# Performance work log

Hardware: AMD Instinct MI355X
Metric: run time of the kernel (lower is better)

Reference implementation:

```python
import jax, jax.numpy as jnp
import numpy as np

EPS = 1e-6
H = 16; D_NOPE = 128; D_ROPE = 64; D_V = 128; D_QK = D_NOPE + D_ROPE
Q_RANK = 1536; KV_RANK = 512; HID = 2048


def rmsnorm(x, w):
    var = jnp.mean(jnp.square(x.astype(jnp.float32)), axis=-1, keepdims=True)
    return (x * jax.lax.rsqrt(var + EPS)).astype(x.dtype) * w


def rotate_half(x):
    x1, x2 = jnp.split(x, 2, axis=-1)
    return jnp.concatenate([-x2, x1], axis=-1)


def interleave(x):
    # deepseek interleaved rope: pairs (0,1),(2,3).. -> [evens | odds]
    b, h, s, d = x.shape
    return x.reshape(b, h, s, d // 2, 2).transpose(0, 1, 2, 4, 3).reshape(b, h, s, d)


def setup_inputs() -> dict:
    key = jax.random.key(0)
    ks = jax.random.split(key, 8)
    B, S = 2, 2048
    sc = lambda n: 1.0 / np.sqrt(n)
    inp = {
        'hidden_states': jax.random.normal(ks[0], (B, S, HID), jnp.float32),
        'w_qa': jax.random.normal(ks[1], (HID, Q_RANK), jnp.float32) * sc(HID),
        'g_qa': jnp.ones((Q_RANK,), jnp.float32),
        'w_qb': jax.random.normal(ks[2], (Q_RANK, H * D_QK), jnp.float32) * sc(Q_RANK),
        'w_kva': jax.random.normal(ks[3], (HID, KV_RANK + D_ROPE), jnp.float32) * sc(HID),
        'g_kva': jnp.ones((KV_RANK,), jnp.float32),
        'w_kvb': jax.random.normal(ks[4], (KV_RANK, H * (D_NOPE + D_V)), jnp.float32) * sc(KV_RANK),
        'w_o': jax.random.normal(ks[5], (H * D_V, HID), jnp.float32) * sc(H * D_V),
    }
    pos = jnp.arange(S, dtype=jnp.float32)
    inv = 1.0 / (10000.0 ** (jnp.arange(0, D_ROPE, 2, dtype=jnp.float32) / D_ROPE))
    emb = jnp.concatenate([pos[:, None] * inv[None, :]] * 2, axis=-1)  # [S, 64]
    inp['cos'] = jnp.broadcast_to(jnp.cos(emb)[None], (B, S, D_ROPE))
    inp['sin'] = jnp.broadcast_to(jnp.sin(emb)[None], (B, S, D_ROPE))
    return inp


def reference(hidden_states, w_qa, g_qa, w_qb, w_kva, g_kva, w_kvb, w_o, cos, sin):
    B, S, _ = hidden_states.shape
    scaling = D_QK ** -0.5
    # low-rank Q: q_b_proj(q_a_layernorm(q_a_proj(h)))
    q = rmsnorm(hidden_states @ w_qa, g_qa) @ w_qb
    q = q.reshape(B, S, H, D_QK).transpose(0, 2, 1, 3)          # [B,H,S,192]
    q_pass, q_rot = q[..., :D_NOPE], q[..., D_NOPE:]
    # compressed KV latent + shared rope key
    ckv = hidden_states @ w_kva                                  # [B,S,576]
    k_pass, k_rot = ckv[..., :KV_RANK], ckv[..., KV_RANK:]
    kv = rmsnorm(k_pass, g_kva) @ w_kvb                          # [B,S,H*256]
    kv = kv.reshape(B, S, H, D_NOPE + D_V).transpose(0, 2, 1, 3)
    k_nope, v = kv[..., :D_NOPE], kv[..., D_NOPE:]
    k_rot = k_rot.reshape(B, 1, S, D_ROPE)
    c = cos[:, None, :, :]; sn = sin[:, None, :, :]
    q_rot = interleave(q_rot); k_rot = interleave(k_rot)
    q_rot = q_rot * c + rotate_half(q_rot) * sn
    k_rot = k_rot * c + rotate_half(k_rot) * sn
    k_rot = jnp.broadcast_to(k_rot, (B, H, S, D_ROPE))
    qf = jnp.concatenate([q_pass, q_rot], axis=-1)               # [B,H,S,192]
    kf = jnp.concatenate([k_nope, k_rot], axis=-1)               # [B,H,S,192]
    scores = jnp.einsum('bhqd,bhkd->bhqk', qf, kf) * scaling
    mask = jnp.triu(jnp.full((S, S), jnp.finfo(jnp.float32).min, jnp.float32), 1)
    probs = jax.nn.softmax(scores.astype(jnp.float32) + mask, axis=-1).astype(qf.dtype)
    out = jnp.einsum('bhqk,bhkd->bhqd', probs, v)                # [B,H,S,128]
    out = out.transpose(0, 2, 1, 3).reshape(B, S, H * D_V)
    return out @ w_o
```

## Files before the change

kernel.cpp:

```cpp
#include <hip/hip_runtime.h>

#define DI __device__ __forceinline__

typedef __attribute__((ext_vector_type(8))) unsigned short u16x8;
typedef __attribute__((ext_vector_type(8))) __bf16 bf16x8;
typedef __attribute__((ext_vector_type(4))) float f32x4;

constexpr int B_ = 2, S_ = 2048, H_ = 16, HID_ = 2048;
constexpr int QR = 1536, KVR = 512, DQK = 192;
constexpr int BS = B_ * S_;
constexpr float SCALE = 0.07216878364870323f;
constexpr float QS = SCALE * 1.4426950408889634f;
constexpr int CKV_LD = 2176;

DI unsigned short f2bf(float x){
  unsigned r;
  asm("v_cvt_pk_bf16_f32 %0, %1, %2" : "=v"(r) : "v"(x), "v"(x));
  return (unsigned short)r;
}
DI float bf2f(unsigned short h){
  return __builtin_bit_cast(float, ((unsigned)h) << 16);
}
DI f32x4 mfma16(u16x8 a, u16x8 b, f32x4 c){
  return __builtin_amdgcn_mfma_f32_16x16x32_bf16(
      __builtin_bit_cast(bf16x8, a), __builtin_bit_cast(bf16x8, b), c, 0, 0, 0);
}
DI void async16(const void* g, void* l){
  __builtin_amdgcn_global_load_lds(
      (__attribute__((address_space(1))) void*)(g),
      (__attribute__((address_space(3))) void*)(l), 16, 0, 0);
}

__global__ __launch_bounds__(256) void cvt_f32_bf16(const float* __restrict__ in,
                                                    unsigned short* __restrict__ out, int n8){
  const int i = blockIdx.x * 256 + threadIdx.x;
  if (i >= n8) return;
  const float4* pp = (const float4*)in + (long)i * 2;
  float4 a = pp[0], b = pp[1];
  u16x8 r;
  r[0]=f2bf(a.x); r[1]=f2bf(a.y); r[2]=f2bf(a.z); r[3]=f2bf(a.w);
  r[4]=f2bf(b.x); r[5]=f2bf(b.y); r[6]=f2bf(b.z); r[7]=f2bf(b.w);
  *(u16x8*)(out + (long)i * 8) = r;
}

__global__ __launch_bounds__(256) void wtrans(const float* __restrict__ W,
                                              unsigned short* __restrict__ Wt,
                                              int K, int N, int Np){
  __shared__ float t[32][33];
  const int n0 = blockIdx.x * 32, k0 = blockIdx.y * 32;
  const int tid = threadIdx.x;
  const int c = tid & 31, r0 = tid >> 5;
  #pragma unroll
  for (int i = 0; i < 4; ++i){
    const int r = r0 + i * 8;
    float v = 0.f;
    if (n0 + c < N) v = W[(long)(k0 + r) * N + n0 + c];
    t[r][c] = v;
  }
  __syncthreads();
  #pragma unroll
  for (int i = 0; i < 4; ++i){
    const int r = r0 + i * 8;
    Wt[(long)(n0 + r) * K + k0 + c] = f2bf(t[c][r]);
  }
}

template<int COLS>
__global__ __launch_bounds__(256) void rmsnorm_k(const float* __restrict__ X, int ldx,
                                                 const float* __restrict__ g,
                                                 unsigned short* __restrict__ Y, int ldy){
  constexpr int PT = COLS / 256;
  const int row = blockIdx.x, tid = threadIdx.x;
  const float* xr = X + (long)row * ldx;
  float v[PT];
  float ss = 0.f;
  #pragma unroll
  for (int i = 0; i < PT; ++i){ v[i] = xr[tid + i * 256]; ss += v[i] * v[i]; }
  #pragma unroll
  for (int off = 32; off >= 1; off >>= 1) ss += __shfl_xor(ss, off);
  __shared__ float red[4];
  if ((tid & 63) == 0) red[tid >> 6] = ss;
  __syncthreads();
  const float tot = red[0] + red[1] + red[2] + red[3];
  const float rs = rsqrtf(tot / (float)COLS + 1e-6f);
  #pragma unroll
  for (int i = 0; i < PT; ++i)
    Y[(long)row * ldy + tid + i * 256] = f2bf(v[i] * rs * g[tid + i * 256]);
}

__global__ __launch_bounds__(256) void gemm_bt(const unsigned short* __restrict__ A,
                                               const unsigned short* __restrict__ Bt,
                                               float* __restrict__ C, int N, int K){
  __shared__ unsigned short lA[128 * 64];
  __shared__ unsigned short lB[128 * 64];
  const int tid = threadIdx.x;
  const int w = tid >> 6, lane = tid & 63, lr = lane & 15, lg = lane >> 4;
  const int wm = w >> 1, wn = w & 1;
  const long m0 = (long)blockIdx.y * 128, n0 = (long)blockIdx.x * 128;
  f32x4 acc[4][4] = {};
  const unsigned short* Ab = A + m0 * K;
  const unsigned short* Bb = Bt + n0 * K;
  for (int k0 = 0; k0 < K; k0 += 64){
    #pragma unroll
    for (int s2 = 0; s2 < 4; ++s2){
      const int c = s2 * 256 + tid;
      async16(Ab + (long)(c >> 3) * K + k0 + (c & 7) * 8, &lA[(s2 * 256 + w * 64) * 8]);
      async16(Bb + (long)(c >> 3) * K + k0 + (c & 7) * 8, &lB[(s2 * 256 + w * 64) * 8]);
    }
    __syncthreads();
    u16x8 a[2][4], b[2][4];
    #pragma unroll
    for (int kk = 0; kk < 2; ++kk){
      #pragma unroll
      for (int m = 0; m < 4; ++m)
        a[kk][m] = *(const u16x8*)&lA[(wm * 64 + m * 16 + lr) * 64 + kk * 32 + lg * 8];
      #pragma unroll
      for (int n = 0; n < 4; ++n)
        b[kk][n] = *(const u16x8*)&lB[(wn * 64 + n * 16 + lr) * 64 + kk * 32 + lg * 8];
    }
    #pragma unroll
    for (int kk = 0; kk < 2; ++kk)
      #pragma unroll
      for (int m = 0; m < 4; ++m)
        #pragma unroll
        for (int n = 0; n < 4; ++n)
          acc[m][n] = mfma16(a[kk][m], b[kk][n], acc[m][n]);
    __syncthreads();
  }
  #pragma unroll
  for (int m = 0; m < 4; ++m){
    const long row = m0 + wm * 64 + m * 16 + lg * 4;
    #pragma unroll
    for (int n = 0; n < 4; ++n){
      const long col = n0 + wn * 64 + n * 16 + lr;
      #pragma unroll
      for (int r = 0; r < 4; ++r)
        C[(row + r) * N + col] = acc[m][n][r];
    }
  }
}

__global__ __launch_bounds__(256) void gemm_qpack(const unsigned short* __restrict__ A,
                                                  const unsigned short* __restrict__ Bt,
                                                  const float* __restrict__ cosb,
                                                  const float* __restrict__ sinb,
                                                  unsigned short* __restrict__ qf, int K){
  const int N = 3072;
  __shared__ unsigned short lA[128 * 64];
  __shared__ unsigned short lB[128 * 64];
  const int tid = threadIdx.x;
  const int w = tid >> 6, lane = tid & 63, lr = lane & 15, lg = lane >> 4;
  const int wm = w >> 1, wn = w & 1;
  const long m0 = (long)blockIdx.y * 128, n0 = (long)blockIdx.x * 128;
  f32x4 acc[4][4] = {};
  const unsigned short* Ab = A + m0 * K;
  const unsigned short* Bb = Bt + n0 * K;
  for (int k0 = 0; k0 < K; k0 += 64){
    #pragma unroll
    for (int s2 = 0; s2 < 4; ++s2){
      const int c = s2 * 256 + tid;
      async16(Ab + (long)(c >> 3) * K + k0 + (c & 7) * 8, &lA[(s2 * 256 + w * 64) * 8]);
      async16(Bb + (long)(c >> 3) * K + k0 + (c & 7) * 8, &lB[(s2 * 256 + w * 64) * 8]);
    }
    __syncthreads();
    u16x8 a[2][4], b[2][4];
    #pragma unroll
    for (int kk = 0; kk < 2; ++kk){
      #pragma unroll
      for (int m = 0; m < 4; ++m)
        a[kk][m] = *(const u16x8*)&lA[(wm * 64 + m * 16 + lr) * 64 + kk * 32 + lg * 8];
      #pragma unroll
      for (int n = 0; n < 4; ++n)
        b[kk][n] = *(const u16x8*)&lB[(wn * 64 + n * 16 + lr) * 64 + kk * 32 + lg * 8];
    }
    #pragma unroll
    for (int kk = 0; kk < 2; ++kk)
      #pragma unroll
      for (int m = 0; m < 4; ++m)
        #pragma unroll
        for (int n = 0; n < 4; ++n)
          acc[m][n] = mfma16(a[kk][m], b[kk][n], acc[m][n]);
    __syncthreads();
  }
  #pragma unroll
  for (int m = 0; m < 4; ++m){
    const int rowg = (int)m0 + wm * 64 + m * 16 + lg * 4;
    #pragma unroll
    for (int n = 0; n < 4; ++n){
      const int col = (int)n0 + wn * 64 + n * 16 + lr;
      const int h = (unsigned)col / 192u;
      const int d = col - h * 192;
      #pragma unroll
      for (int r = 0; r < 4; ++r){
        const int rowi = rowg + r;
        const float a = acc[m][n][r];
        const float partner = __shfl_xor(a, 1);
        float val; int dout;
        if (d < 128){ val = a; dout = d; }
        else {
          const int ii = (d - 128) >> 1;
          const float c  = cosb[(long)rowi * 64 + ii];
          const float sn = sinb[(long)rowi * 64 + ii];
          val  = (d & 1) ? (a * c + partner * sn) : (a * c - partner * sn);
          dout = 128 + ((d & 1) << 5) + ii;
        }
        const int b = rowi >> 11, s = rowi & 2047;
        qf[((long)(b * 16 + h) * S_ + s) * DQK + dout] = f2bf(val * QS);
      }
    }
  }
}

__global__ __launch_bounds__(256) void gemm_kvpack(const unsigned short* __restrict__ A,
                                                   const unsigned short* __restrict__ Bt,
                                                   unsigned short* __restrict__ kf,
                                                   unsigned short* __restrict__ kvm, int K){
  const int N = 4096;
  __shared__ unsigned short lA[128 * 64];
  __shared__ unsigned short lB[128 * 64];
  const int tid = threadIdx.x;
  const int w = tid >> 6, lane = tid & 63, lr = lane & 15, lg = lane >> 4;
  const int wm = w >> 1, wn = w & 1;
  const long m0 = (long)blockIdx.y * 128, n0 = (long)blockIdx.x * 128;
  f32x4 acc[4][4] = {};
  const unsigned short* Ab = A + m0 * K;
  const unsigned short* Bb = Bt + n0 * K;
  for (int k0 = 0; k0 < K; k0 += 64){
    #pragma unroll
    for (int s2 = 0; s2 < 4; ++s2){
      const int c = s2 * 256 + tid;
      async16(Ab + (long)(c >> 3) * K + k0 + (c & 7) * 8, &lA[(s2 * 256 + w * 64) * 8]);
      async16(Bb + (long)(c >> 3) * K + k0 + (c & 7) * 8, &lB[(s2 * 256 + w * 64) * 8]);
    }
    __syncthreads();
    u16x8 a[2][4], b[2][4];
    #pragma unroll
    for (int kk = 0; kk < 2; ++kk){
      #pragma unroll
      for (int m = 0; m < 4; ++m)
        a[kk][m] = *(const u16x8*)&lA[(wm * 64 + m * 16 + lr) * 64 + kk * 32 + lg * 8];
      #pragma unroll
      for (int n = 0; n < 4; ++n)
        b[kk][n] = *(const u16x8*)&lB[(wn * 64 + n * 16 + lr) * 64 + kk * 32 + lg * 8];
    }
    #pragma unroll
    for (int kk = 0; kk < 2; ++kk)
      #pragma unroll
      for (int m = 0; m < 4; ++m)
        #pragma unroll
        for (int n = 0; n < 4; ++n)
          acc[m][n] = mfma16(a[kk][m], b[kk][n], acc[m][n]);
    __syncthreads();
  }
  #pragma unroll
  for (int m = 0; m < 4; ++m){
    const int rowg = (int)m0 + wm * 64 + m * 16 + lg * 4;
    #pragma unroll
    for (int n = 0; n < 4; ++n){
      const int col = (int)n0 + wn * 64 + n * 16 + lr;
      const int h = col >> 8, d = col & 255;
      #pragma unroll
      for (int r = 0; r < 4; ++r){
        const int rowi = rowg + r;
        const unsigned short v = f2bf(acc[m][n][r]);
        const int b = rowi >> 11, s = rowi & 2047;
        if (d < 128) kf[((long)(b * 16 + h) * S_ + s) * DQK + d] = v;
        else         kvm[(long)rowi * 4096 + col] = v;
      }
    }
  }
}

__global__ __launch_bounds__(256) void pack_krot(const float* __restrict__ ckv,
                                                 const float* __restrict__ cosb,
                                                 const float* __restrict__ sinb,
                                                 unsigned short* __restrict__ kf){
  const int row = blockIdx.x, tid = threadIdx.x;
  const int b = row >> 11, s = row & 2047;
  const float* cv = ckv + (long)row * CKV_LD + QR + KVR;
  const float* cr = cosb + (long)row * 64;
  const float* sr = sinb + (long)row * 64;
  #pragma unroll
  for (int j = 0; j < 4; ++j){
    const int o = j * 256 + tid;
    const int h = o >> 6, i = o & 63, ii = i & 31;
    const float e = cv[2 * ii], od = cv[2 * ii + 1];
    const float c = cr[ii], sn = sr[ii];
    const float val = (i < 32) ? (e * c - od * sn) : (od * c + e * sn);
    kf[((long)(b * 16 + h) * S_ + s) * DQK + 128 + i] = f2bf(val);
  }
}

__global__ __launch_bounds__(256) void pack_v(const unsigned short* __restrict__ kvm,
                                              unsigned short* __restrict__ vt){
  const int bh = blockIdx.x, s0 = blockIdx.y * 64;
  const int b = bh >> 4, h = bh & 15;
  __shared__ unsigned short t[64][130];
  #pragma unroll
  for (int it = 0; it < 32; ++it){
    const int idx = it * 256 + threadIdx.x;
    const int sl = idx >> 7, d = idx & 127;
    t[sl][d] = kvm[(long)(b * S_ + s0 + sl) * 4096 + h * 256 + 128 + d];
  }
  __syncthreads();
  #pragma unroll
  for (int it = 0; it < 32; ++it){
    const int idx = it * 256 + threadIdx.x;
    const int dr = idx >> 6, sc = idx & 63;
    vt[(long)(bh * 128 + dr) * S_ + s0 + sc] = t[sc][dr];
  }
}

__global__ __launch_bounds__(256) void mla_attn(const unsigned short* __restrict__ qf,
                                                const unsigned short* __restrict__ kf,
                                                const unsigned short* __restrict__ vt,
                                                unsigned short* __restrict__ ao){
  __shared__ unsigned short k_lds[2][64 * 192];
  __shared__ unsigned short v_lds[2][128 * 64];
  __shared__ unsigned short p_lds[4][32][72];
  const int bid = blockIdx.x;
  const int u = bid >> 5;
  const int qt = (u < 8) ? (15 - u) : (u - 8);
  const int bh = bid & 31;
  const int b = bh >> 4, h = bh & 15;
  const int tid = threadIdx.x;
  const int w = tid >> 6, lane = tid & 63, lr = lane & 15, lg = lane >> 4;
  const int q0 = qt * 128 + w * 32;
  const unsigned short* qb = qf + (long)bh * S_ * DQK;
  const unsigned short* kb = kf + (long)bh * S_ * DQK;
  const unsigned short* vb = vt + (long)bh * 128 * S_;
  u16x8 aq[2][6];
  #pragma unroll
  for (int mi = 0; mi < 2; ++mi)
    #pragma unroll
    for (int kk = 0; kk < 6; ++kk)
      aq[mi][kk] = *(const u16x8*)&qb[(long)(q0 + mi * 16 + lr) * DQK + kk * 32 + lg * 8];
  f32x4 oacc[2][8] = {};
  f32x4 lacc[2] = {};
  float mrun[2][4];
  #pragma unroll
  for (int mi = 0; mi < 2; ++mi)
    #pragma unroll
    for (int r = 0; r < 4; ++r) mrun[mi][r] = -1e30f;
  u16x8 onesv;
  #pragma unroll
  for (int i = 0; i < 8; ++i) onesv[i] = 0x3F80;
  const int ktiles = (qt + 1) * 2;
  const int myktiles = ((q0 + 31) >> 6) + 1;

  auto stage = [&](int kt, int buf){
    #pragma unroll
    for (int s2 = 0; s2 < 6; ++s2){
      const int c = s2 * 256 + tid;
      const int row = c / 24, col = c - row * 24;
      async16(kb + (long)(kt * 64 + row) * DQK + ((col ^ (row & 7)) << 3),
              &k_lds[buf][(s2 * 256 + w * 64) * 8]);
    }
    #pragma unroll
    for (int s2 = 0; s2 < 4; ++s2){
      const int c = s2 * 256 + tid;
      const int row = c >> 3, col = c & 7;
      async16(vb + (long)row * S_ + kt * 64 + ((col ^ (row & 7)) << 3),
              &v_lds[buf][(s2 * 256 + w * 64) * 8]);
    }
  };

  stage(0, 0);
  __syncthreads();
  int cur = 0;
  for (int kt = 0; kt < ktiles; ++kt){
    if (kt + 1 < ktiles) stage(kt + 1, cur ^ 1);
    if (kt < myktiles){
      f32x4 sacc[2][4] = {};
      #pragma unroll
      for (int ni = 0; ni < 4; ++ni){
        const int rowk = ni * 16 + lr;
        #pragma unroll
        for (int kk = 0; kk < 6; ++kk){
          const int col16 = kk * 4 + lg;
          const u16x8 bk = *(const u16x8*)&k_lds[cur][rowk * 192 + ((col16 ^ (rowk & 7)) << 3)];
          sacc[0][ni] = mfma16(aq[0][kk], bk, sacc[0][ni]);
          sacc[1][ni] = mfma16(aq[1][kk], bk, sacc[1][ni]);
        }
      }
      const int kbase = kt * 64;
      if (kbase + 63 > q0){
        #pragma unroll
        for (int mi = 0; mi < 2; ++mi)
          #pragma unroll
          for (int r = 0; r < 4; ++r){
            const int qrow = q0 + mi * 16 + lg * 4 + r;
            #pragma unroll
            for (int ni = 0; ni < 4; ++ni)
              if (kbase + ni * 16 + lr > qrow) sacc[mi][ni][r] = -1e30f;
          }
      }
      #pragma unroll
      for (int mi = 0; mi < 2; ++mi)
        #pragma unroll
        for (int r = 0; r < 4; ++r){
          float tm = fmaxf(fmaxf(sacc[mi][0][r], sacc[mi][1][r]),
                           fmaxf(sacc[mi][2][r], sacc[mi][3][r]));
          tm = fmaxf(tm, __shfl_xor(tm, 1));
          tm = fmaxf(tm, __shfl_xor(tm, 2));
          tm = fmaxf(tm, __shfl_xor(tm, 4));
          tm = fmaxf(tm, __shfl_xor(tm, 8));
          if (tm > mrun[mi][r] + 8.f){
            const float sc = __builtin_exp2f(mrun[mi][r] - tm);
            mrun[mi][r] = tm;
            lacc[mi][r] *= sc;
            #pragma unroll
            for (int d = 0; d < 8; ++d) oacc[mi][d][r] *= sc;
          }
          const float m_ = mrun[mi][r];
          const int qq = mi * 16 + lg * 4 + r;
          p_lds[w][qq][lr]      = f2bf(__builtin_exp2f(sacc[mi][0][r] - m_));
          p_lds[w][qq][16 + lr] = f2bf(__builtin_exp2f(sacc[mi][1][r] - m_));
          p_lds[w][qq][32 + lr] = f2bf(__builtin_exp2f(sacc[mi][2][r] - m_));
          p_lds[w][qq][48 + lr] = f2bf(__builtin_exp2f(sacc[mi][3][r] - m_));
        }
      u16x8 pa[2][2];
      #pragma unroll
      for (int mi = 0; mi < 2; ++mi)
        #pragma unroll
        for (int kk2 = 0; kk2 < 2; ++kk2)
          pa[mi][kk2] = *(const u16x8*)&p_lds[w][mi * 16 + lr][kk2 * 32 + lg * 8];
      #pragma unroll
      for (int mi = 0; mi < 2; ++mi)
        #pragma unroll
        for (int kk2 = 0; kk2 < 2; ++kk2)
          lacc[mi] = mfma16(pa[mi][kk2], onesv, lacc[mi]);
      #pragma unroll
      for (int d = 0; d < 8; ++d){
        const int rowv = d * 16 + lr;
        #pragma unroll
        for (int kk2 = 0; kk2 < 2; ++kk2){
          const int col16 = kk2 * 4 + lg;
          const u16x8 bv = *(const u16x8*)&v_lds[cur][rowv * 64 + ((col16 ^ (rowv & 7)) << 3)];
          oacc[0][d] = mfma16(pa[0][kk2], bv, oacc[0][d]);
          oacc[1][d] = mfma16(pa[1][kk2], bv, oacc[1][d]);
        }
      }
    }
    __syncthreads();
    cur ^= 1;
  }
  #pragma unroll
  for (int mi = 0; mi < 2; ++mi)
    #pragma unroll
    for (int r = 0; r < 4; ++r){
      const long row = q0 + mi * 16 + lg * 4 + r;
      const float inv = 1.0f / lacc[mi][r];
      #pragma unroll
      for (int d = 0; d < 8; ++d)
        ao[(long)(b * S_ + row) * 2048 + h * 128 + d * 16 + lr] = f2bf(oacc[mi][d][r] * inv);
    }
}

extern "C" void kernel_launch(void* const* d_in, const int* in_sizes, int n_in,
                              void* d_out, int out_size, void* d_ws, size_t ws_size,
                              hipStream_t stream){
  const float* hid   = (const float*)d_in[0];
  const float* w_qa  = (const float*)d_in[1];
  const float* g_qa  = (const float*)d_in[2];
  const float* w_qb  = (const float*)d_in[3];
  const float* w_kva = (const float*)d_in[4];
  const float* g_kva = (const float*)d_in[5];
  const float* w_kvb = (const float*)d_in[6];
  const float* w_o   = (const float*)d_in[7];
  const float* cosb  = (const float*)d_in[8];
  const float* sinb  = (const float*)d_in[9];
  float* out = (float*)d_out;

  char* p = (char*)d_ws;
  auto alloc = [&](size_t bytes) -> void* {
    void* r = p;
    p += (bytes + 255) & ~(size_t)255;
    return r;
  };
  unsigned short* hb      = (unsigned short*)alloc((size_t)BS * HID_ * 2);
  unsigned short* wqakv_t = (unsigned short*)alloc((size_t)CKV_LD * HID_ * 2);
  unsigned short* wqa_t   = wqakv_t;
  unsigned short* wkva_t  = wqakv_t + (size_t)QR * HID_;
  unsigned short* wqb_t  = (unsigned short*)alloc((size_t)3072 * QR * 2);
  unsigned short* wkvb_t = (unsigned short*)alloc((size_t)4096 * KVR * 2);
  unsigned short* wo_t   = (unsigned short*)alloc((size_t)2048 * 2048 * 2);
  float*          qakv_f = (float*)alloc((size_t)BS * CKV_LD * 4);
  unsigned short* qan    = (unsigned short*)alloc((size_t)BS * QR * 2);
  unsigned short* kvn    = (unsigned short*)alloc((size_t)BS * KVR * 2);
  unsigned short* kvmat  = (unsigned short*)alloc((size_t)BS * 4096 * 2);
  unsigned short* qfb    = (unsigned short*)alloc((size_t)32 * S_ * DQK * 2);
  unsigned short* kfb    = (unsigned short*)alloc((size_t)32 * S_ * DQK * 2);
  unsigned short* vtb    = (unsigned short*)alloc((size_t)32 * 128 * S_ * 2);
  unsigned short* aob    = (unsigned short*)alloc((size_t)BS * 2048 * 2);
  (void)ws_size; (void)in_sizes; (void)n_in; (void)out_size;

  cvt_f32_bf16<<<BS * HID_ / 8 / 256, 256, 0, stream>>>(hid, hb, BS * HID_ / 8);
  wtrans<<<dim3(1536 / 32, 2048 / 32), 256, 0, stream>>>(w_qa, wqa_t, 2048, 1536, 1536);
  wtrans<<<dim3(3072 / 32, 1536 / 32), 256, 0, stream>>>(w_qb, wqb_t, 1536, 3072, 3072);
  wtrans<<<dim3(640 / 32, 2048 / 32), 256, 0, stream>>>(w_kva, wkva_t, 2048, 576, 640);
  wtrans<<<dim3(4096 / 32, 512 / 32), 256, 0, stream>>>(w_kvb, wkvb_t, 512, 4096, 4096);
  wtrans<<<dim3(2048 / 32, 2048 / 32), 256, 0, stream>>>(w_o, wo_t, 2048, 2048, 2048);

  gemm_bt<<<dim3(CKV_LD / 128, BS / 128), 256, 0, stream>>>(hb, wqakv_t, qakv_f, CKV_LD, 2048);
  rmsnorm_k<1536><<<BS, 256, 0, stream>>>(qakv_f, CKV_LD, g_qa, qan, 1536);
  rmsnorm_k<512><<<BS, 256, 0, stream>>>(qakv_f + QR, CKV_LD, g_kva, kvn, 512);

  gemm_qpack<<<dim3(3072 / 128, BS / 128), 256, 0, stream>>>(qan, wqb_t, cosb, sinb, qfb, 1536);
  gemm_kvpack<<<dim3(4096 / 128, BS / 128), 256, 0, stream>>>(kvn, wkvb_t, kfb, kvmat, 512);
  pack_krot<<<BS, 256, 0, stream>>>(qakv_f, cosb, sinb, kfb);
  pack_v<<<dim3(32, S_ / 64), 256, 0, stream>>>(kvmat, vtb);

  mla_attn<<<512, 256, 0, stream>>>(qfb, kfb, vtb, aob);

  gemm_bt<<<dim3(2048 / 128, BS / 128), 256, 0, stream>>>(aob, wo_t, out, 2048, 2048);
}
```

Before: 637.6 us.

## Shrink attention query tile to 64 rows and drop double buffering

```diff
diff --git a/kernel.cpp b/kernel.cpp
--- a/kernel.cpp
+++ b/kernel.cpp
@@ -315,146 +315,116 @@
                                                 const unsigned short* __restrict__ kf,
                                                 const unsigned short* __restrict__ vt,
                                                 unsigned short* __restrict__ ao){
-  __shared__ unsigned short k_lds[2][64 * 192];
-  __shared__ unsigned short v_lds[2][128 * 64];
-  __shared__ unsigned short p_lds[4][32][72];
+  __shared__ unsigned short k_lds[64 * 192];
+  __shared__ unsigned short v_lds[128 * 64];
+  __shared__ unsigned short p_lds[4][16][72];
   const int bid = blockIdx.x;
   const int u = bid >> 5;
-  const int qt = (u < 8) ? (15 - u) : (u - 8);
+  const int qt = 31 - u;
   const int bh = bid & 31;
   const int b = bh >> 4, h = bh & 15;
   const int tid = threadIdx.x;
   const int w = tid >> 6, lane = tid & 63, lr = lane & 15, lg = lane >> 4;
-  const int q0 = qt * 128 + w * 32;
+  const int q0 = qt * 64 + w * 16;
   const unsigned short* qb = qf + (long)bh * S_ * DQK;
   const unsigned short* kb = kf + (long)bh * S_ * DQK;
   const unsigned short* vb = vt + (long)bh * 128 * S_;
-  u16x8 aq[2][6];
-  #pragma unroll
-  for (int mi = 0; mi < 2; ++mi)
-    #pragma unroll
-    for (int kk = 0; kk < 6; ++kk)
-      aq[mi][kk] = *(const u16x8*)&qb[(long)(q0 + mi * 16 + lr) * DQK + kk * 32 + lg * 8];
-  f32x4 oacc[2][8] = {};
-  f32x4 lacc[2] = {};
-  float mrun[2][4];
-  #pragma unroll
-  for (int mi = 0; mi < 2; ++mi)
-    #pragma unroll
-    for (int r = 0; r < 4; ++r) mrun[mi][r] = -1e30f;
+  u16x8 aq[6];
+  #pragma unroll
+  for (int kk = 0; kk < 6; ++kk)
+    aq[kk] = *(const u16x8*)&qb[(long)(q0 + lr) * DQK + kk * 32 + lg * 8];
+  f32x4 oacc[8] = {};
+  f32x4 lacc = {};
+  float mrun[4] = {-1e30f, -1e30f, -1e30f, -1e30f};
   u16x8 onesv;
   #pragma unroll
   for (int i = 0; i < 8; ++i) onesv[i] = 0x3F80;
-  const int ktiles = (qt + 1) * 2;
-  const int myktiles = ((q0 + 31) >> 6) + 1;
-
-  auto stage = [&](int kt, int buf){
+  const int ktiles = qt + 1;
+  for (int kt = 0; kt < ktiles; ++kt){
     #pragma unroll
     for (int s2 = 0; s2 < 6; ++s2){
       const int c = s2 * 256 + tid;
       const int row = c / 24, col = c - row * 24;
       async16(kb + (long)(kt * 64 + row) * DQK + ((col ^ (row & 7)) << 3),
-              &k_lds[buf][(s2 * 256 + w * 64) * 8]);
+              &k_lds[(s2 * 256 + w * 64) * 8]);
     }
     #pragma unroll
     for (int s2 = 0; s2 < 4; ++s2){
       const int c = s2 * 256 + tid;
       const int row = c >> 3, col = c & 7;
       async16(vb + (long)row * S_ + kt * 64 + ((col ^ (row & 7)) << 3),
-              &v_lds[buf][(s2 * 256 + w * 64) * 8]);
-    }
-  };
-
-  stage(0, 0);
-  __syncthreads();
-  int cur = 0;
-  for (int kt = 0; kt < ktiles; ++kt){
-    if (kt + 1 < ktiles) stage(kt + 1, cur ^ 1);
-    if (kt < myktiles){
-      f32x4 sacc[2][4] = {};
-      #pragma unroll
-      for (int ni = 0; ni < 4; ++ni){
-        const int rowk = ni * 16 + lr;
+              &v_lds[(s2 * 256 + w * 64) * 8]);
+    }
+    __syncthreads();
+    f32x4 sacc[4] = {};
+    #pragma unroll
+    for (int ni = 0; ni < 4; ++ni){
+      const int rowk = ni * 16 + lr;
+      #pragma unroll
+      for (int kk = 0; kk < 6; ++kk){
+        const int col16 = kk * 4 + lg;
+        const u16x8 bk = *(const u16x8*)&k_lds[rowk * 192 + ((col16 ^ (rowk & 7)) << 3)];
+        sacc[ni] = mfma16(aq[kk], bk, sacc[ni]);
+      }
+    }
+    if (kt == qt){
+      #pragma unroll
+      for (int r = 0; r < 4; ++r){
+        const int qloc = w * 16 + lg * 4 + r;
         #pragma unroll
-        for (int kk = 0; kk < 6; ++kk){
-          const int col16 = kk * 4 + lg;
-          const u16x8 bk = *(const u16x8*)&k_lds[cur][rowk * 192 + ((col16 ^ (rowk & 7)) << 3)];
-          sacc[0][ni] = mfma16(aq[0][kk], bk, sacc[0][ni]);
-          sacc[1][ni] = mfma16(aq[1][kk], bk, sacc[1][ni]);
-        }
-      }
-      const int kbase = kt * 64;
-      if (kbase + 63 > q0){
+        for (int ni = 0; ni < 4; ++ni)
+          if (ni * 16 + lr > qloc) sacc[ni][r] = -1e30f;
+      }
+    }
+    #pragma unroll
+    for (int r = 0; r < 4; ++r){
+      float tm = fmaxf(fmaxf(sacc[0][r], sacc[1][r]),
+                       fmaxf(sacc[2][r], sacc[3][r]));
+      tm = fmaxf(tm, __shfl_xor(tm, 1));
+      tm = fmaxf(tm, __shfl_xor(tm, 2));
+      tm = fmaxf(tm, __shfl_xor(tm, 4));
+      tm = fmaxf(tm, __shfl_xor(tm, 8));
+      if (tm > mrun[r] + 8.f){
+        const float sc = __builtin_exp2f(mrun[r] - tm);
+        mrun[r] = tm;
+        lacc[r] *= sc;
         #pragma unroll
-        for (int mi = 0; mi < 2; ++mi)
-          #pragma unroll
-          for (int r = 0; r < 4; ++r){
-            const int qrow = q0 + mi * 16 + lg * 4 + r;
-            #pragma unroll
-            for (int ni = 0; ni < 4; ++ni)
-              if (kbase + ni * 16 + lr > qrow) sacc[mi][ni][r] = -1e30f;
-          }
-      }
-      #pragma unroll
-      for (int mi = 0; mi < 2; ++mi)
-        #pragma unroll
-        for (int r = 0; r < 4; ++r){
-          float tm = fmaxf(fmaxf(sacc[mi][0][r], sacc[mi][1][r]),
-                           fmaxf(sacc[mi][2][r], sacc[mi][3][r]));
-          tm = fmaxf(tm, __shfl_xor(tm, 1));
-          tm = fmaxf(tm, __shfl_xor(tm, 2));
-          tm = fmaxf(tm, __shfl_xor(tm, 4));
-          tm = fmaxf(tm, __shfl_xor(tm, 8));
-          if (tm > mrun[mi][r] + 8.f){
-            const float sc = __builtin_exp2f(mrun[mi][r] - tm);
-            mrun[mi][r] = tm;
-            lacc[mi][r] *= sc;
-            #pragma unroll
-            for (int d = 0; d < 8; ++d) oacc[mi][d][r] *= sc;
-          }
-          const float m_ = mrun[mi][r];
-          const int qq = mi * 16 + lg * 4 + r;
-          p_lds[w][qq][lr]      = f2bf(__builtin_exp2f(sacc[mi][0][r] - m_));
-          p_lds[w][qq][16 + lr] = f2bf(__builtin_exp2f(sacc[mi][1][r] - m_));
-          p_lds[w][qq][32 + lr] = f2bf(__builtin_exp2f(sacc[mi][2][r] - m_));
-          p_lds[w][qq][48 + lr] = f2bf(__builtin_exp2f(sacc[mi][3][r] - m_));
-        }
-      u16x8 pa[2][2];
-      #pragma unroll
-      for (int mi = 0; mi < 2; ++mi)
-        #pragma unroll
-        for (int kk2 = 0; kk2 < 2; ++kk2)
-          pa[mi][kk2] = *(const u16x8*)&p_lds[w][mi * 16 + lr][kk2 * 32 + lg * 8];
-      #pragma unroll
-      for (int mi = 0; mi < 2; ++mi)
-        #pragma unroll
-        for (int kk2 = 0; kk2 < 2; ++kk2)
-          lacc[mi] = mfma16(pa[mi][kk2], onesv, lacc[mi]);
-      #pragma unroll
-      for (int d = 0; d < 8; ++d){
-        const int rowv = d * 16 + lr;
-        #pragma unroll
-        for (int kk2 = 0; kk2 < 2; ++kk2){
-          const int col16 = kk2 * 4 + lg;
-          const u16x8 bv = *(const u16x8*)&v_lds[cur][rowv * 64 + ((col16 ^ (rowv & 7)) << 3)];
-          oacc[0][d] = mfma16(pa[0][kk2], bv, oacc[0][d]);
-          oacc[1][d] = mfma16(pa[1][kk2], bv, oacc[1][d]);
-        }
-      }
-    }
-    __syncthreads();
-    cur ^= 1;
-  }
-  #pragma unroll
-  for (int mi = 0; mi < 2; ++mi)
-    #pragma unroll
-    for (int r = 0; r < 4; ++r){
-      const long row = q0 + mi * 16 + lg * 4 + r;
-      const float inv = 1.0f / lacc[mi][r];
-      #pragma unroll
-      for (int d = 0; d < 8; ++d)
-        ao[(long)(b * S_ + row) * 2048 + h * 128 + d * 16 + lr] = f2bf(oacc[mi][d][r] * inv);
-    }
+        for (int d = 0; d < 8; ++d) oacc[d][r] *= sc;
+      }
+      const float m_ = mrun[r];
+      const int qq = lg * 4 + r;
+      p_lds[w][qq][lr]      = f2bf(__builtin_exp2f(sacc[0][r] - m_));
+      p_lds[w][qq][16 + lr] = f2bf(__builtin_exp2f(sacc[1][r] - m_));
+      p_lds[w][qq][32 + lr] = f2bf(__builtin_exp2f(sacc[2][r] - m_));
+      p_lds[w][qq][48 + lr] = f2bf(__builtin_exp2f(sacc[3][r] - m_));
+    }
+    u16x8 pa[2];
+    #pragma unroll
+    for (int kk2 = 0; kk2 < 2; ++kk2)
+      pa[kk2] = *(const u16x8*)&p_lds[w][lr][kk2 * 32 + lg * 8];
+    #pragma unroll
+    for (int kk2 = 0; kk2 < 2; ++kk2)
+      lacc = mfma16(pa[kk2], onesv, lacc);
+    #pragma unroll
+    for (int d = 0; d < 8; ++d){
+      const int rowv = d * 16 + lr;
+      #pragma unroll
+      for (int kk2 = 0; kk2 < 2; ++kk2){
+        const int col16 = kk2 * 4 + lg;
+        const u16x8 bv = *(const u16x8*)&v_lds[rowv * 64 + ((col16 ^ (rowv & 7)) << 3)];
+        oacc[d] = mfma16(pa[kk2], bv, oacc[d]);
+      }
+    }
+    __syncthreads();
+  }
+  #pragma unroll
+  for (int r = 0; r < 4; ++r){
+    const long row = q0 + lg * 4 + r;
+    const float inv = 1.0f / lacc[r];
+    #pragma unroll
+    for (int d = 0; d < 8; ++d)
+      ao[(long)(b * S_ + row) * 2048 + h * 128 + d * 16 + lr] = f2bf(oacc[d][r] * inv);
+  }
 }
 
 extern "C" void kernel_launch(void* const* d_in, const int* in_sizes, int n_in,
@@ -511,7 +481,7 @@
   pack_krot<<<BS, 256, 0, stream>>>(qakv_f, cosb, sinb, kfb);
   pack_v<<<dim3(32, S_ / 64), 256, 0, stream>>>(kvmat, vtb);
 
-  mla_attn<<<512, 256, 0, stream>>>(qfb, kfb, vtb, aob);
+  mla_attn<<<1024, 256, 0, stream>>>(qfb, kfb, vtb, aob);
 
   gemm_bt<<<dim3(2048 / 128, BS / 128), 256, 0, stream>>>(aob, wo_t, out, 2048, 2048);
 }
```

Result: faster. 551.8 us (-13.5%).
